# Kernel optimization log

Measured on AMD Instinct MI355X. Metric: run time of the kernel, lower is better.

Reference implementation:

```python
import jax, jax.numpy as jnp
import numpy as np

DILATION = 6
KS = 3
N = KS * KS  # 9 kernel sample points
PAD = 1      # zero padding inside DeformConv2d
EPS = 1e-5


def conv2d(x, w, b=None, padding=0):
    out = jax.lax.conv_general_dilated(
        x, w, window_strides=(1, 1),
        padding=[(padding, padding), (padding, padding)],
        dimension_numbers=('NCHW', 'OIHW', 'NCHW'))
    if b is not None:
        out = out + b[None, :, None, None]
    return out


def batchnorm_train(x, gamma, beta):
    # training-mode BN (module default): batch statistics over (N,H,W)
    mean = x.mean(axis=(0, 2, 3), keepdims=True)
    var = x.var(axis=(0, 2, 3), keepdims=True)
    return gamma[None, :, None, None] * (x - mean) * jax.lax.rsqrt(var + EPS) + beta[None, :, None, None]


def deform_conv(x, p_w, p_b, m_w, m_b, d_w, d_b, w):
    b, c, h, wd = x.shape
    offset = conv2d(x, p_w, p_b, padding=1)                 # (b, 2N, h, w)
    m = jax.nn.sigmoid(conv2d(x, m_w, m_b, padding=1))      # (b, N, h, w) modulation
    s = 2.0 * jax.nn.sigmoid(conv2d(x, d_w, d_b, padding=1))  # (b,1,h,w) adaptive dilation scale (=1 at logit 0)
    xp = jnp.pad(x, ((0, 0), (0, 0), (PAD, PAD), (PAD, PAD)))
    Hp, Wp = h + 2 * PAD, wd + 2 * PAD
    # kernel grid p_n, row-major (kh, kw) to match conv weight layout
    rng = jnp.arange(-(KS - 1) // 2, (KS - 1) // 2 + 1, dtype=x.dtype)
    pn_x, pn_y = jnp.meshgrid(rng, rng, indexing='ij')
    pn_x, pn_y = pn_x.reshape(-1), pn_y.reshape(-1)          # (N,)
    # base sampling positions (offset by PAD into padded map)
    p0_x = jnp.arange(1, h + 1, dtype=x.dtype)[:, None, None]    # (h,1,1)
    p0_y = jnp.arange(1, wd + 1, dtype=x.dtype)[None, :, None]   # (1,w,1)
    off = offset.transpose(0, 2, 3, 1)   # (b,h,w,2N)
    s_ = s.transpose(0, 2, 3, 1)         # (b,h,w,1)
    px = p0_x + DILATION * s_ * pn_x + off[..., :N]   # (b,h,w,N)
    py = p0_y + DILATION * s_ * pn_y + off[..., N:]
    fx, fy = jnp.floor(px), jnp.floor(py)
    qx_lt = jnp.clip(fx, 0, Hp - 1).astype(jnp.int32)
    qy_lt = jnp.clip(fy, 0, Wp - 1).astype(jnp.int32)
    qx_rb = jnp.clip(fx + 1, 0, Hp - 1).astype(jnp.int32)
    qy_rb = jnp.clip(fy + 1, 0, Wp - 1).astype(jnp.int32)
    pxc = jnp.clip(px, 0, Hp - 1)
    pyc = jnp.clip(py, 0, Wp - 1)
    g_lt = (1 + (qx_lt - pxc)) * (1 + (qy_lt - pyc))
    g_rb = (1 - (qx_rb - pxc)) * (1 - (qy_rb - pyc))
    g_lb = (1 + (qx_lt - pxc)) * (1 - (qy_rb - pyc))
    g_rt = (1 - (qx_rb - pxc)) * (1 + (qy_lt - pyc))

    def gather(qx, qy):
        idx = (qx * Wp + qy).reshape(b, 1, -1)                    # (b,1,h*w*N)
        xf = xp.reshape(b, c, Hp * Wp)
        out = jnp.take_along_axis(xf, jnp.broadcast_to(idx, (b, c, idx.shape[-1])), axis=2)
        return out.reshape(b, c, h, wd, N)

    x_off = (g_lt[:, None] * gather(qx_lt, qy_lt)
             + g_rb[:, None] * gather(qx_rb, qy_rb)
             + g_lb[:, None] * gather(qx_lt, qy_rb)
             + g_rt[:, None] * gather(qx_rb, qy_lt))
    x_off = x_off * m.transpose(0, 2, 3, 1)[:, None]              # modulation
    # final 3x3 conv over gathered samples == contraction over (c, N)
    return jnp.einsum('bchwn,ocn->bohw', x_off, w.reshape(w.shape[0], c, N))


def setup_inputs() -> dict:
    key = jax.random.key(0)
    ks = jax.random.split(key, 12)
    cin, c1, c2 = 512, 256, 64
    b, h, w = 2, 96, 96
    def rn(k, shape, scale):
        return jax.random.normal(k, shape, dtype=jnp.float32) * scale
    return {
        'x': rn(ks[0], (b, cin, h, w), 1.0),
        'bn1_g': jnp.ones((cin,), jnp.float32),
        'bn1_b': jnp.zeros((cin,), jnp.float32),
        'conv1_w': rn(ks[1], (c1, cin, 1, 1), (1.0 / cin) ** 0.5),
        'conv1_b': jnp.zeros((c1,), jnp.float32),
        'bn2_g': jnp.ones((c1,), jnp.float32),
        'bn2_b': jnp.zeros((c1,), jnp.float32),
        'p_w': rn(ks[2], (2 * N, c1, 3, 3), 0.01),
        'p_b': jnp.zeros((2 * N,), jnp.float32),
        'm_w': rn(ks[3], (N, c1, 3, 3), 0.01),
        'm_b': jnp.zeros((N,), jnp.float32),
        'd_w': rn(ks[4], (1, c1, 3, 3), 0.01),
        'd_b': jnp.zeros((1,), jnp.float32),
        'dconv_w': rn(ks[5], (c2, c1, 3, 3), (1.0 / (c1 * 9)) ** 0.5),
    }


def reference(x, bn1_g, bn1_b, conv1_w, conv1_b, bn2_g, bn2_b,
              p_w, p_b, m_w, m_b, d_w, d_b, dconv_w):
    f = jax.nn.relu(batchnorm_train(x, bn1_g, bn1_b))
    f = conv2d(f, conv1_w, conv1_b)
    f = batchnorm_train(f, bn2_g, bn2_b)
    return deform_conv(f, p_w, p_b, m_w, m_b, d_w, d_b, dconv_w)
```

## Files before the change

### kernel.cpp

```cpp
#include <hip/hip_runtime.h>
#include <hip/hip_bf16.h>
#include <math.h>

#define BATCH 2
#define CIN 512
#define C1 256
#define C2 64
#define HH 96
#define WW 96
#define HWSZ 9216
#define NPIX 18432
#define HP 98
#define WP 98

typedef __attribute__((ext_vector_type(8))) short bf16x8;
typedef __attribute__((ext_vector_type(4))) short bf16x4;
typedef __attribute__((ext_vector_type(4))) float f32x4;
typedef __attribute__((ext_vector_type(4))) unsigned int u32x4;
typedef __attribute__((ext_vector_type(2))) unsigned int u32x2;
typedef unsigned short u16;
typedef unsigned int u32;

__device__ __forceinline__ float bfu2f(u16 u) {
  u32 v = ((u32)u) << 16; return __builtin_bit_cast(float, v);
}
__device__ __forceinline__ u16 f2bfu(float f) {
  return __builtin_bit_cast(u16, __float2bfloat16(f));
}
__device__ __forceinline__ float rd_any(const void* p, size_t i, int fl) {
  return fl ? bfu2f(((const u16*)p)[i]) : ((const float*)p)[i];
}
__device__ __forceinline__ int get_fl(const u32* g1raw) {
  return g1raw[0] != 0x3F800000u;
}
__device__ __forceinline__ bf16x8 lds_frag(const u16* p) {
  bf16x4 lo = *(const bf16x4*)p;
  bf16x4 hi = *(const bf16x4*)(p + 4);
  bf16x8 r;
  r[0] = lo[0]; r[1] = lo[1]; r[2] = lo[2]; r[3] = lo[3];
  r[4] = hi[0]; r[5] = hi[1]; r[6] = hi[2]; r[7] = hi[3];
  return r;
}
__device__ __forceinline__ void split4(const f32x4& v, u32x2& ph, u32x2& pl) {
  u16 h0 = f2bfu(v[0]), h1 = f2bfu(v[1]), h2 = f2bfu(v[2]), h3 = f2bfu(v[3]);
  u16 l0 = f2bfu(v[0] - bfu2f(h0)), l1 = f2bfu(v[1] - bfu2f(h1));
  u16 l2 = f2bfu(v[2] - bfu2f(h2)), l3 = f2bfu(v[3] - bfu2f(h3));
  ph = (u32x2){(u32)h0 | ((u32)h1 << 16), (u32)h2 | ((u32)h3 << 16)};
  pl = (u32x2){(u32)l0 | ((u32)l1 << 16), (u32)l2 | ((u32)l3 << 16)};
}

#define PREP_BASE 356380
#define NOPART 589824
#define NOUT 1179648
#define NBORD 198656

__global__ __launch_bounds__(256) void prep_kernel(
    const void* cw, const void* pw, const void* mw, const void* dw, const void* dcw,
    const void* cb, const void* g1, const void* b1, const void* g2, const void* b2,
    const void* pb, const void* mb, const void* db,
    u16* __restrict__ W1b, u16* __restrict__ W1l,
    u16* __restrict__ Wofa, u16* __restrict__ Wofal,
    u16* __restrict__ Wab, u16* __restrict__ Wabl,
    float* __restrict__ canon, float* __restrict__ statz,
    float* __restrict__ opartZ, float* __restrict__ oscrZ, void* __restrict__ outZ,
    float* __restrict__ xpfB, int nextra) {
  int e = blockIdx.x * 256 + threadIdx.x;
  if (e >= PREP_BASE + nextra) return;
  int fl = get_fl((const u32*)g1);
  if (e < 131072) {
    float v = rd_any(cw, e, fl);
    u16 h = f2bfu(v);
    W1b[e] = h; W1l[e] = f2bfu(v - bfu2f(h));
  } else if (e < 204800) {
    int i = e - 131072;
    int tap = i >> 13; int r = i & 8191; int m = r >> 8; int c = r & 255;
    float v = 0.f;
    if (m < 18)       v = rd_any(pw, (size_t)(m * 256 + c) * 9 + tap, fl);
    else if (m < 27)  v = rd_any(mw, (size_t)((m - 18) * 256 + c) * 9 + tap, fl);
    else if (m == 27) v = rd_any(dw, (size_t)c * 9 + tap, fl);
    u16 h = f2bfu(v);
    Wofa[i] = h; Wofal[i] = f2bfu(v - bfu2f(h));
  } else if (e < 352256) {
    int i = e - 204800;
    int n = i >> 14; int r = i & 16383; int o = r >> 8; int c = r & 255;
    float v = rd_any(dcw, (size_t)(o * 256 + c) * 9 + n, fl);
    u16 h = f2bfu(v);
    Wab[i] = h; Wabl[i] = f2bfu(v - bfu2f(h));
  } else if (e < 354076) {
    int i = e - 352256;
    const void* src; int off;
    if      (i < 256)  { src = cb; off = i; }
    else if (i < 768)  { src = g1; off = i - 256; }
    else if (i < 1280) { src = b1; off = i - 768; }
    else if (i < 1536) { src = g2; off = i - 1280; }
    else if (i < 1792) { src = b2; off = i - 1536; }
    else if (i < 1810) { src = pb; off = i - 1792; }
    else if (i < 1819) { src = mb; off = i - 1810; }
    else               { src = db; off = i - 1819; }
    canon[i] = rd_any(src, off, fl);
  } else if (e < PREP_BASE) {
    statz[e - 354076] = 0.f;
  } else {
    int k = e - PREP_BASE;
    if (k < NOPART) {
      opartZ[k] = 0.f;
    } else if (k < NOPART + NOUT) {
      int i = k - NOPART;
      if (fl) { ((u16*)outZ)[i] = 0; oscrZ[i] = 0.f; }
      else    { ((float*)outZ)[i] = 0.f; }
    } else {
      int i = k - NOPART - NOUT;
      int ch = i & 255; int pxi = i >> 8;
      int bb = pxi / 388; int r = pxi % 388;
      int h, w;
      if (r < 98)      { h = 0;  w = r; }
      else if (r < 196){ h = 97; w = r - 98; }
      else if (r < 292){ h = r - 196 + 1; w = 0; }
      else             { h = r - 292 + 1; w = 97; }
      xpfB[(((size_t)(bb * HP) + h) * WP + w) * C1 + ch] = 0.f;
    }
  }
}

__global__ __launch_bounds__(256) void init_kernel(
    const u32* __restrict__ g1raw, void* __restrict__ outv,
    float* __restrict__ oscr, float* __restrict__ opart, float* __restrict__ xpf) {
  int i = blockIdx.x * 256 + threadIdx.x;
  if (i < NOUT) {
    if (get_fl(g1raw)) { ((u16*)outv)[i] = 0; oscr[i] = 0.f; }
    else               { ((float*)outv)[i] = 0.f; }
  } else if (i < NOUT + NOPART) {
    opart[i - NOUT] = 0.f;
  } else {
    int k = i - NOUT - NOPART;
    int ch = k & 255; int pxi = k >> 8;
    int bb = pxi / 388; int r = pxi % 388;
    int h, w;
    if (r < 98)      { h = 0;  w = r; }
    else if (r < 196){ h = 97; w = r - 98; }
    else if (r < 292){ h = r - 196 + 1; w = 0; }
    else             { h = r - 292 + 1; w = 97; }
    xpf[(((size_t)(bb * HP) + h) * WP + w) * C1 + ch] = 0.f;
  }
}

__global__ __launch_bounds__(256) void bn_stats_kernel(
    const void* __restrict__ x, const float* __restrict__ gamma,
    const float* __restrict__ beta, float* __restrict__ scale,
    float* __restrict__ shift, float* __restrict__ sums, float* __restrict__ sumsq,
    int* __restrict__ cnt, const u32* __restrict__ g1raw, int C) {
  int c = blockIdx.x, part = blockIdx.y, tid = threadIdx.x;
  int fl = get_fl(g1raw);
  int b = part >> 1, half = part & 1;
  size_t base = ((size_t)(b * C + c)) * HWSZ + half * (HWSZ / 2);
  float s = 0.f, q = 0.f;
  if (fl) {
    const u16* p = (const u16*)x + base;
    for (int i = tid; i < 576; i += 256) {
      u32x4 U = *(const u32x4*)(p + i * 8);
      #pragma unroll
      for (int k = 0; k < 4; ++k) {
        float v0 = bfu2f((u16)(U[k] & 0xffff));
        float v1 = bfu2f((u16)(U[k] >> 16));
        s += v0 + v1; q = fmaf(v0, v0, fmaf(v1, v1, q));
      }
    }
  } else {
    const float* p = (const float*)x + base;
    for (int i = tid; i < 1152; i += 256) {
      f32x4 v = *(const f32x4*)(p + i * 4);
      #pragma unroll
      for (int k = 0; k < 4; ++k) { s += v[k]; q = fmaf(v[k], v[k], q); }
    }
  }
  __shared__ float sh[512];
  sh[tid] = s; sh[tid + 256] = q;
  __syncthreads();
  for (int off = 128; off > 0; off >>= 1) {
    if (tid < off) { sh[tid] += sh[tid + off]; sh[tid + 256] += sh[tid + 256 + off]; }
    __syncthreads();
  }
  if (tid == 0) {
    atomicAdd(&sums[c], sh[0]);
    atomicAdd(&sumsq[c], sh[256]);
    __threadfence();
    int old = atomicAdd(&cnt[c], 1);
    if (old == 3) {
      float S = atomicAdd(&sums[c], 0.f);
      float Q = atomicAdd(&sumsq[c], 0.f);
      float mean = S * (1.f / (float)NPIX);
      float var  = fmaxf(Q * (1.f / (float)NPIX) - mean * mean, 0.f);
      float sc = gamma[c] * rsqrtf(var + 1e-5f);
      scale[c] = sc;
      shift[c] = beta[c] - mean * sc;
    }
  }
}

__global__ __launch_bounds__(256) void conv1x1_kernel(
    const void* __restrict__ x, const u16* __restrict__ W1b, const u16* __restrict__ W1l,
    const float* __restrict__ cb, const float* __restrict__ scale,
    const float* __restrict__ shift, const u32* __restrict__ g1raw,
    u16* __restrict__ f1, float* __restrict__ sums2, float* __restrict__ sumsq2) {
  __shared__ u16 Bh[64][68];
  __shared__ u16 Bl[64][68];
  int tid = threadIdx.x;
  int fl = get_fl(g1raw);
  int bxr = blockIdx.x;
  int bx = (bxr & 7) * 36 + (bxr >> 3);
  int p0 = bx * 64;
  int b = p0 / HWSZ;
  int hw0 = p0 % HWSZ;
  int lane = tid & 63, wv = tid >> 6, quad = lane >> 4, mr = lane & 15;
  int m0 = wv * 64;
  f32x4 acc[4][4];
  #pragma unroll
  for (int i = 0; i < 4; ++i)
    #pragma unroll
    for (int j = 0; j < 4; ++j) acc[i][j] = (f32x4){0.f, 0.f, 0.f, 0.f};

  int spx = tid & 63, cg = tid >> 6;
  int gpx = hw0 + spx;
  for (int c0 = 0; c0 < CIN; c0 += 64) {
    __syncthreads();
    #pragma unroll
    for (int j = 0; j < 8; ++j) {
      int ci = c0 + cg * 16 + j * 2;
      float v0, v1;
      if (fl) {
        const u16* xb = (const u16*)x;
        v0 = bfu2f(xb[((size_t)(b * CIN + ci)) * HWSZ + gpx]);
        v1 = bfu2f(xb[((size_t)(b * CIN + ci + 1)) * HWSZ + gpx]);
      } else {
        const float* xf = (const float*)x;
        v0 = xf[((size_t)(b * CIN + ci)) * HWSZ + gpx];
        v1 = xf[((size_t)(b * CIN + ci + 1)) * HWSZ + gpx];
      }
      v0 = fmaxf(fmaf(v0, scale[ci], shift[ci]), 0.f);
      v1 = fmaxf(fmaf(v1, scale[ci + 1], shift[ci + 1]), 0.f);
      u16 h0 = f2bfu(v0), h1 = f2bfu(v1);
      u16 l0 = f2bfu(v0 - bfu2f(h0)), l1 = f2bfu(v1 - bfu2f(h1));
      *(u32*)&Bh[spx][cg * 16 + j * 2] = (u32)h0 | ((u32)h1 << 16);
      *(u32*)&Bl[spx][cg * 16 + j * 2] = (u32)l0 | ((u32)l1 << 16);
    }
    __syncthreads();
    #pragma unroll
    for (int kk2 = 0; kk2 < 2; ++kk2) {
      int kk = kk2 * 32;
      #pragma unroll
      for (int mf = 0; mf < 4; ++mf) {
        size_t wix = (size_t)(m0 + mf * 16 + mr) * CIN + c0 + kk + quad * 8;
        bf16x8 ah = *(const bf16x8*)(W1b + wix);
        bf16x8 al = *(const bf16x8*)(W1l + wix);
        #pragma unroll
        for (int nt = 0; nt < 4; ++nt) {
          bf16x8 bl = lds_frag(&Bl[nt * 16 + mr][kk + quad * 8]);
          bf16x8 bh = lds_frag(&Bh[nt * 16 + mr][kk + quad * 8]);
          acc[mf][nt] = __builtin_amdgcn_mfma_f32_16x16x32_bf16(ah, bl, acc[mf][nt], 0, 0, 0);
          acc[mf][nt] = __builtin_amdgcn_mfma_f32_16x16x32_bf16(al, bh, acc[mf][nt], 0, 0, 0);
          acc[mf][nt] = __builtin_amdgcn_mfma_f32_16x16x32_bf16(ah, bh, acc[mf][nt], 0, 0, 0);
        }
      }
    }
  }
  #pragma unroll
  for (int mf = 0; mf < 4; ++mf) {
    #pragma unroll
    for (int r = 0; r < 4; ++r) {
      int co = m0 + mf * 16 + quad * 4 + r;
      float bi = cb[co];
      float sv = 0.f, sq = 0.f;
      #pragma unroll
      for (int nt = 0; nt < 4; ++nt) {
        float v = acc[mf][nt][r] + bi;
        f1[((size_t)(b * C1 + co)) * HWSZ + hw0 + nt * 16 + mr] = f2bfu(v);
        sv += v; sq = fmaf(v, v, sq);
      }
      #pragma unroll
      for (int m = 1; m < 16; m <<= 1) {
        sv += __shfl_xor(sv, m);
        sq += __shfl_xor(sq, m);
      }
      if (mr == 0) {
        atomicAdd(&sums2[co], sv);
        atomicAdd(&sumsq2[co], sq);
      }
    }
  }
}

__global__ __launch_bounds__(256) void bn2pad_kernel(
    const u16* __restrict__ f1, const float* __restrict__ sums2,
    const float* __restrict__ sumsq2, const float* __restrict__ g2c,
    const float* __restrict__ b2c, float* __restrict__ xpf) {
  int bid = blockIdx.x;
  int ht = bid % 144; int ct = (bid / 144) & 3; int b = bid / 576;
  int hw0 = ht * 64, c0 = ct * 64;
  __shared__ float t[64][65];
  __shared__ float s2[64], sh2[64];
  int tid = threadIdx.x;
  if (tid < 64) {
    int c = c0 + tid;
    float S = sums2[c], Q = sumsq2[c];
    float mean = S * (1.f / (float)NPIX);
    float var  = fmaxf(Q * (1.f / (float)NPIX) - mean * mean, 0.f);
    float sc = g2c[c] * rsqrtf(var + 1e-5f);
    s2[tid] = sc;
    sh2[tid] = b2c[c] - mean * sc;
  }
  __syncthreads();
  #pragma unroll
  for (int it = 0; it < 16; ++it) {
    int e = it * 256 + tid;
    int p = e & 63, ci = e >> 6;
    float v = bfu2f(f1[((size_t)(b * C1 + c0 + ci)) * HWSZ + hw0 + p]);
    t[ci][p] = fmaf(v, s2[ci], sh2[ci]);
  }
  __syncthreads();
  #pragma unroll
  for (int it = 0; it < 16; ++it) {
    int e = it * 256 + tid;
    int ci = e & 63, p = e >> 6;
    int hw = hw0 + p; int h = hw / WW; int w = hw % WW;
    xpf[(((size_t)(b * HP) + h + 1) * WP + w + 1) * C1 + c0 + ci] = t[ci][p];
  }
}

__global__ __launch_bounds__(256) void offconv_kernel(
    const float* __restrict__ xpf, const u16* __restrict__ Wofa, const u16* __restrict__ Wofal,
    const float* __restrict__ pbc, const float* __restrict__ mbc,
    const float* __restrict__ dbc, float* __restrict__ opart) {
  __shared__ u16 Vh[32][68];
  __shared__ u16 Vl[32][68];
  int tid = threadIdx.x;
  int bxr = blockIdx.x;
  int bx = (bxr & 7) * 72 + (bxr >> 3);
  int tg = blockIdx.y;
  int p0 = bx * 32;
  int b = p0 / HWSZ;
  int hw = p0 % HWSZ; int h0 = hw / WW; int w0 = hw % WW;
  int lane = tid & 63, wv = tid >> 6, quad = lane >> 4, mr = lane & 15;
  int m0 = (wv & 1) * 16;
  int ntile = wv >> 1;
  int srow = tid >> 4;
  int scol = (tid & 15) * 4;
  f32x4 acc = (f32x4){0.f, 0.f, 0.f, 0.f};
  for (int tt = 0; tt < 3; ++tt) {
    int tap = tg * 3 + tt;
    int th = tap / 3, tw = tap % 3;
    const float* base = xpf + ((size_t)(b * HP + h0 + th) * WP + (w0 + tw)) * C1;
    for (int c0i = 0; c0i < 4; ++c0i) {
      int c0 = c0i * 64;
      if (tt | c0i) __syncthreads();
      #pragma unroll
      for (int pass = 0; pass < 2; ++pass) {
        int px = pass * 16 + srow;
        f32x4 v = *(const f32x4*)(base + (size_t)px * C1 + c0 + scol);
        u32x2 ph, pl;
        split4(v, ph, pl);
        *(u32x2*)&Vh[px][scol] = ph;
        *(u32x2*)&Vl[px][scol] = pl;
      }
      __syncthreads();
      #pragma unroll
      for (int kk2 = 0; kk2 < 2; ++kk2) {
        int kof = kk2 * 32 + quad * 8;
        size_t wix = (size_t)(tap * 32 + m0 + mr) * C1 + c0 + kof;
        bf16x8 ah = *(const bf16x8*)(Wofa + wix);
        bf16x8 al = *(const bf16x8*)(Wofal + wix);
        bf16x8 bl = lds_frag(&Vl[ntile * 16 + mr][kof]);
        bf16x8 bh = lds_frag(&Vh[ntile * 16 + mr][kof]);
        acc = __builtin_amdgcn_mfma_f32_16x16x32_bf16(ah, bl, acc, 0, 0, 0);
        acc = __builtin_amdgcn_mfma_f32_16x16x32_bf16(al, bh, acc, 0, 0, 0);
        acc = __builtin_amdgcn_mfma_f32_16x16x32_bf16(ah, bh, acc, 0, 0, 0);
      }
    }
  }
  int px = ntile * 16 + mr;
  #pragma unroll
  for (int r = 0; r < 4; ++r) {
    int m = m0 + quad * 4 + r;
    if (m < 28) {
      float v = acc[r];
      if (tg == 0) v += (m < 18) ? pbc[m] : ((m < 27) ? mbc[m - 18] : dbc[0]);
      atomicAdd(&opart[(size_t)m * NPIX + p0 + px], v);
    }
  }
}

__global__ __launch_bounds__(256) void deform_kernel(
    const float* __restrict__ xpf, const u16* __restrict__ Wab, const u16* __restrict__ Wabl,
    const float* __restrict__ opart, const u32* __restrict__ g1raw,
    float* __restrict__ oscr, void* __restrict__ outv) {
  __shared__ u16   Vh[64][68];
  __shared__ u16   Vl[64][68];
  __shared__ int   smi[4][64];
  __shared__ float smw[4][64];
  int tid = threadIdx.x;
  int bxr = blockIdx.x;
  int bx = (bxr & 7) * 36 + (bxr >> 3);
  int n = blockIdx.y;
  int p0 = bx * 64;
  int b = p0 / HWSZ;
  int hw0 = p0 % HWSZ;

  if (tid < 64) {
    int p = tid;
    int bp = p0 + p;
    int hw = hw0 + p; int h = hw / WW; int w = hw % WW;
    float offx = opart[(size_t)n * NPIX + bp];
    float offy = opart[(size_t)(9 + n) * NPIX + bp];
    float mlog = opart[(size_t)(18 + n) * NPIX + bp];
    float slog = opart[(size_t)27 * NPIX + bp];
    float mm = 1.f / (1.f + expf(-mlog));
    float s  = 2.f / (1.f + expf(-slog));
    float pnx = (float)(n / 3 - 1), pny = (float)(n % 3 - 1);
    float px = (float)(h + 1) + 6.f * s * pnx + offx;
    float py = (float)(w + 1) + 6.f * s * pny + offy;
    float fx = floorf(px), fy = floorf(py);
    float qxlt = fminf(fmaxf(fx, 0.f), 97.f);
    float qylt = fminf(fmaxf(fy, 0.f), 97.f);
    float qxrb = fminf(fmaxf(fx + 1.f, 0.f), 97.f);
    float qyrb = fminf(fmaxf(fy + 1.f, 0.f), 97.f);
    float pxc = fminf(fmaxf(px, 0.f), 97.f);
    float pyc = fminf(fmaxf(py, 0.f), 97.f);
    float glt = (1.f + (qxlt - pxc)) * (1.f + (qylt - pyc));
    float grb = (1.f - (qxrb - pxc)) * (1.f - (qyrb - pyc));
    float glb = (1.f + (qxlt - pxc)) * (1.f - (qyrb - pyc));
    float grt = (1.f - (qxrb - pxc)) * (1.f + (qylt - pyc));
    int ixlt = (int)qxlt, iylt = (int)qylt, ixrb = (int)qxrb, iyrb = (int)qyrb;
    int base = b * (HP * WP);
    smi[0][p] = base + ixlt * WP + iylt;  smw[0][p] = glt * mm;
    smi[1][p] = base + ixrb * WP + iyrb;  smw[1][p] = grb * mm;
    smi[2][p] = base + ixlt * WP + iyrb;  smw[2][p] = glb * mm;
    smi[3][p] = base + ixrb * WP + iylt;  smw[3][p] = grt * mm;
  }
  __syncthreads();

  int lane = tid & 63, wv = tid >> 6, quad = lane >> 4, mr = lane & 15;
  int m0 = wv * 16;
  int srow = tid >> 4;
  int scol = (tid & 15) * 4;
  f32x4 acc[4];
  #pragma unroll
  for (int i = 0; i < 4; ++i) acc[i] = (f32x4){0.f, 0.f, 0.f, 0.f};

  const float* bp[4][4];
  float wt[4][4];
  #pragma unroll
  for (int pass = 0; pass < 4; ++pass) {
    int px = pass * 16 + srow;
    #pragma unroll
    for (int c = 0; c < 4; ++c) {
      bp[pass][c] = xpf + (size_t)smi[c][px] * C1 + scol;
      wt[pass][c] = smw[c][px];
    }
  }
  f32x4 pv[4][4];
  #pragma unroll
  for (int pass = 0; pass < 4; ++pass)
    #pragma unroll
    for (int c = 0; c < 4; ++c) pv[pass][c] = *(const f32x4*)(bp[pass][c]);

  for (int c0i = 0; c0i < 4; ++c0i) {
    int c0 = c0i * 64;
    if (c0i) __syncthreads();
    #pragma unroll
    for (int pass = 0; pass < 4; ++pass) {
      int px = pass * 16 + srow;
      f32x4 vc;
      #pragma unroll
      for (int j = 0; j < 4; ++j)
        vc[j] = fmaf(wt[pass][0], pv[pass][0][j],
                 fmaf(wt[pass][1], pv[pass][1][j],
                  fmaf(wt[pass][2], pv[pass][2][j], wt[pass][3] * pv[pass][3][j])));
      u32x2 ph, pl;
      split4(vc, ph, pl);
      *(u32x2*)&Vh[px][scol] = ph;
      *(u32x2*)&Vl[px][scol] = pl;
    }
    __syncthreads();
    if (c0i < 3) {
      int cn = c0 + 64;
      #pragma unroll
      for (int pass = 0; pass < 4; ++pass)
        #pragma unroll
        for (int c = 0; c < 4; ++c) pv[pass][c] = *(const f32x4*)(bp[pass][c] + cn);
    }
    #pragma unroll
    for (int kk2 = 0; kk2 < 2; ++kk2) {
      int kof = kk2 * 32 + quad * 8;
      size_t wix = (size_t)(n * C2 + m0 + mr) * C1 + c0 + kof;
      bf16x8 ah = *(const bf16x8*)(Wab + wix);
      bf16x8 al = *(const bf16x8*)(Wabl + wix);
      #pragma unroll
      for (int nt = 0; nt < 4; ++nt) {
        bf16x8 bl = lds_frag(&Vl[nt * 16 + mr][kof]);
        bf16x8 bh = lds_frag(&Vh[nt * 16 + mr][kof]);
        acc[nt] = __builtin_amdgcn_mfma_f32_16x16x32_bf16(ah, bl, acc[nt], 0, 0, 0);
        acc[nt] = __builtin_amdgcn_mfma_f32_16x16x32_bf16(al, bh, acc[nt], 0, 0, 0);
        acc[nt] = __builtin_amdgcn_mfma_f32_16x16x32_bf16(ah, bh, acc[nt], 0, 0, 0);
      }
    }
  }
  int fl = get_fl(g1raw);
  float* tgt = fl ? oscr : (float*)outv;
  #pragma unroll
  for (int nt = 0; nt < 4; ++nt) {
    #pragma unroll
    for (int r = 0; r < 4; ++r) {
      int o = m0 + quad * 4 + r;
      int hw = hw0 + nt * 16 + mr;
      atomicAdd(&tgt[((size_t)(b * C2 + o)) * HWSZ + hw], acc[nt][r]);
    }
  }
}

__global__ void cvt_out_kernel(const u32* __restrict__ g1raw,
                               const float* __restrict__ oscr, void* __restrict__ outv) {
  if (!get_fl(g1raw)) return;
  int i = blockIdx.x * 256 + threadIdx.x;
  ((u16*)outv)[i] = f2bfu(oscr[i]);
}

extern "C" void kernel_launch(void* const* d_in, const int* in_sizes, int n_in,
                              void* d_out, int out_size, void* d_ws, size_t ws_size,
                              hipStream_t stream) {
  const void* x       = d_in[0];
  const void* bn1_g   = d_in[1];
  const void* bn1_b   = d_in[2];
  const void* conv1_w = d_in[3];
  const void* conv1_b = d_in[4];
  const void* bn2_g   = d_in[5];
  const void* bn2_b   = d_in[6];
  const void* p_w     = d_in[7];
  const void* p_b     = d_in[8];
  const void* m_w     = d_in[9];
  const void* m_b     = d_in[10];
  const void* d_w     = d_in[11];
  const void* d_b     = d_in[12];
  const void* dconv_w = d_in[13];
  const u32* g1raw = (const u32*)bn1_g;

  float* ws = (float*)d_ws;
  float* canon = ws + 16;
  float* cbc = canon + 0;
  float* g1c = canon + 256;
  float* b1c = canon + 768;
  float* g2c = canon + 1280;
  float* b2c = canon + 1536;
  float* pbc = canon + 1792;
  float* mbc = canon + 1810;
  float* dbc = canon + 1819;
  float* scale1 = ws + 1840;
  float* shift1 = ws + 2352;
  float* statz  = ws + 3376;
  float* sums1  = statz;
  float* sumsq1 = statz + 512;
  int*   cnt1   = (int*)(statz + 1024);
  float* sums2  = statz + 1536;
  float* sumsq2 = statz + 1792;
  u16* W1b   = (u16*)(ws + 5680);
  u16* W1l   = (u16*)(ws + 71216);
  u16* Wofa  = (u16*)(ws + 136752);
  u16* Wofal = (u16*)(ws + 173616);
  u16* Wab   = (u16*)(ws + 210480);
  u16* Wabl  = (u16*)(ws + 284208);
  u16* f1    = (u16*)(ws + 357936);

  bool bigws = ws_size >= (size_t)9403952 * 4 + 64;
  float *opart, *oscr, *xpf;
  if (bigws) {
    opart = ws + 2717232;
    oscr  = ws + 3307056;
    xpf   = ws + 4486704;
  } else {
    oscr  = ws + 357936;
    opart = ws + 1537584;
    xpf   = ws + 2717232;
  }

  prep_kernel<<<bigws ? 9081 : 1393, 256, 0, stream>>>(
      conv1_w, p_w, m_w, d_w, dconv_w,
      conv1_b, bn1_g, bn1_b, bn2_g, bn2_b, p_b, m_b, d_b,
      W1b, W1l, Wofa, Wofal, Wab, Wabl, canon, statz,
      opart, oscr, d_out, xpf, bigws ? (NOPART + NOUT + NBORD) : 0);
  bn_stats_kernel<<<dim3(CIN, 4), 256, 0, stream>>>(x, g1c, b1c, scale1, shift1,
                                                    sums1, sumsq1, cnt1, g1raw, CIN);
  conv1x1_kernel<<<288, 256, 0, stream>>>(x, W1b, W1l, cbc, scale1, shift1, g1raw,
                                          f1, sums2, sumsq2);
  bn2pad_kernel<<<1152, 256, 0, stream>>>(f1, sums2, sumsq2, g2c, b2c, xpf);
  if (!bigws)
    init_kernel<<<(NOUT + NOPART + NBORD + 255) / 256, 256, 0, stream>>>(
        g1raw, d_out, oscr, opart, xpf);
  offconv_kernel<<<dim3(576, 3), 256, 0, stream>>>(xpf, Wofa, Wofal, pbc, mbc, dbc, opart);
  deform_kernel<<<dim3(288, 9), 256, 0, stream>>>(xpf, Wab, Wabl, opart, g1raw, oscr, d_out);
  cvt_out_kernel<<<4608, 256, 0, stream>>>(g1raw, oscr, d_out);
}
```

Measured before the change: 339.0 us.

## Retile conv1x1 into smaller blocks with register prefetch; share offconv tap row loads

The 1x1 conv kernel now uses 32-pixel by 128-channel tiles on a 2D grid of 576x2 blocks, four times the previous block count, to raise occupancy. It also prefetches the next input channel slab into registers while the MFMAs run. The offset conv kernel loads one 34-row strip per kernel row and reuses it for all three horizontal taps with shifted LDS reads, which cuts global loads and barriers. In exchange, the conv1x1 input activations are read twice (once per channel half), and more atomics are issued for the BN2 statistics.

```diff
diff --git a/kernel.cpp b/kernel.cpp
--- a/kernel.cpp
+++ b/kernel.cpp
@@ -202,64 +202,68 @@
     const float* __restrict__ cb, const float* __restrict__ scale,
     const float* __restrict__ shift, const u32* __restrict__ g1raw,
     u16* __restrict__ f1, float* __restrict__ sums2, float* __restrict__ sumsq2) {
-  __shared__ u16 Bh[64][68];
-  __shared__ u16 Bl[64][68];
+  __shared__ u16 Bh[32][68];
+  __shared__ u16 Bl[32][68];
   int tid = threadIdx.x;
   int fl = get_fl(g1raw);
   int bxr = blockIdx.x;
-  int bx = (bxr & 7) * 36 + (bxr >> 3);
-  int p0 = bx * 64;
+  int bx = (bxr & 7) * 72 + (bxr >> 3);
+  int p0 = bx * 32;
   int b = p0 / HWSZ;
   int hw0 = p0 % HWSZ;
   int lane = tid & 63, wv = tid >> 6, quad = lane >> 4, mr = lane & 15;
-  int m0 = wv * 64;
-  f32x4 acc[4][4];
-  #pragma unroll
-  for (int i = 0; i < 4; ++i)
-    #pragma unroll
-    for (int j = 0; j < 4; ++j) acc[i][j] = (f32x4){0.f, 0.f, 0.f, 0.f};
-
-  int spx = tid & 63, cg = tid >> 6;
+  int m0 = blockIdx.y * 128 + (wv & 1) * 64;
+  int nt = wv >> 1;
+  f32x4 acc[4];
+  #pragma unroll
+  for (int j = 0; j < 4; ++j) acc[j] = (f32x4){0.f, 0.f, 0.f, 0.f};
+
+  int spx = tid & 31, cg = tid >> 5;
   int gpx = hw0 + spx;
-  for (int c0 = 0; c0 < CIN; c0 += 64) {
-    __syncthreads();
-    #pragma unroll
-    for (int j = 0; j < 8; ++j) {
-      int ci = c0 + cg * 16 + j * 2;
-      float v0, v1;
-      if (fl) {
-        const u16* xb = (const u16*)x;
-        v0 = bfu2f(xb[((size_t)(b * CIN + ci)) * HWSZ + gpx]);
-        v1 = bfu2f(xb[((size_t)(b * CIN + ci + 1)) * HWSZ + gpx]);
-      } else {
-        const float* xf = (const float*)x;
-        v0 = xf[((size_t)(b * CIN + ci)) * HWSZ + gpx];
-        v1 = xf[((size_t)(b * CIN + ci + 1)) * HWSZ + gpx];
-      }
-      v0 = fmaxf(fmaf(v0, scale[ci], shift[ci]), 0.f);
-      v1 = fmaxf(fmaf(v1, scale[ci + 1], shift[ci + 1]), 0.f);
+  const u16* xb = (const u16*)x;
+  const float* xf = (const float*)x;
+  float xv[8];
+  #pragma unroll
+  for (int j = 0; j < 8; ++j) {
+    int ci = cg * 8 + j;
+    xv[j] = fl ? bfu2f(xb[((size_t)(b * CIN + ci)) * HWSZ + gpx])
+               : xf[((size_t)(b * CIN + ci)) * HWSZ + gpx];
+  }
+  for (int c0i = 0; c0i < 8; ++c0i) {
+    int c0 = c0i * 64;
+    if (c0i) __syncthreads();
+    #pragma unroll
+    for (int j = 0; j < 4; ++j) {
+      int ci = c0 + cg * 8 + j * 2;
+      float v0 = fmaxf(fmaf(xv[j * 2], scale[ci], shift[ci]), 0.f);
+      float v1 = fmaxf(fmaf(xv[j * 2 + 1], scale[ci + 1], shift[ci + 1]), 0.f);
       u16 h0 = f2bfu(v0), h1 = f2bfu(v1);
       u16 l0 = f2bfu(v0 - bfu2f(h0)), l1 = f2bfu(v1 - bfu2f(h1));
-      *(u32*)&Bh[spx][cg * 16 + j * 2] = (u32)h0 | ((u32)h1 << 16);
-      *(u32*)&Bl[spx][cg * 16 + j * 2] = (u32)l0 | ((u32)l1 << 16);
+      *(u32*)&Bh[spx][cg * 8 + j * 2] = (u32)h0 | ((u32)h1 << 16);
+      *(u32*)&Bl[spx][cg * 8 + j * 2] = (u32)l0 | ((u32)l1 << 16);
     }
     __syncthreads();
+    if (c0i < 7) {
+      #pragma unroll
+      for (int j = 0; j < 8; ++j) {
+        int ci = c0 + 64 + cg * 8 + j;
+        xv[j] = fl ? bfu2f(xb[((size_t)(b * CIN + ci)) * HWSZ + gpx])
+                   : xf[((size_t)(b * CIN + ci)) * HWSZ + gpx];
+      }
+    }
     #pragma unroll
     for (int kk2 = 0; kk2 < 2; ++kk2) {
-      int kk = kk2 * 32;
+      int kof = kk2 * 32 + quad * 8;
+      bf16x8 bl = lds_frag(&Bl[nt * 16 + mr][kof]);
+      bf16x8 bh = lds_frag(&Bh[nt * 16 + mr][kof]);
       #pragma unroll
       for (int mf = 0; mf < 4; ++mf) {
-        size_t wix = (size_t)(m0 + mf * 16 + mr) * CIN + c0 + kk + quad * 8;
+        size_t wix = (size_t)(m0 + mf * 16 + mr) * CIN + c0 + kof;
         bf16x8 ah = *(const bf16x8*)(W1b + wix);
         bf16x8 al = *(const bf16x8*)(W1l + wix);
-        #pragma unroll
-        for (int nt = 0; nt < 4; ++nt) {
-          bf16x8 bl = lds_frag(&Bl[nt * 16 + mr][kk + quad * 8]);
-          bf16x8 bh = lds_frag(&Bh[nt * 16 + mr][kk + quad * 8]);
-          acc[mf][nt] = __builtin_amdgcn_mfma_f32_16x16x32_bf16(ah, bl, acc[mf][nt], 0, 0, 0);
-          acc[mf][nt] = __builtin_amdgcn_mfma_f32_16x16x32_bf16(al, bh, acc[mf][nt], 0, 0, 0);
-          acc[mf][nt] = __builtin_amdgcn_mfma_f32_16x16x32_bf16(ah, bh, acc[mf][nt], 0, 0, 0);
-        }
+        acc[mf] = __builtin_amdgcn_mfma_f32_16x16x32_bf16(ah, bl, acc[mf], 0, 0, 0);
+        acc[mf] = __builtin_amdgcn_mfma_f32_16x16x32_bf16(al, bh, acc[mf], 0, 0, 0);
+        acc[mf] = __builtin_amdgcn_mfma_f32_16x16x32_bf16(ah, bh, acc[mf], 0, 0, 0);
       }
     }
   }
@@ -268,14 +272,9 @@
     #pragma unroll
     for (int r = 0; r < 4; ++r) {
       int co = m0 + mf * 16 + quad * 4 + r;
-      float bi = cb[co];
-      float sv = 0.f, sq = 0.f;
-      #pragma unroll
-      for (int nt = 0; nt < 4; ++nt) {
-        float v = acc[mf][nt][r] + bi;
-        f1[((size_t)(b * C1 + co)) * HWSZ + hw0 + nt * 16 + mr] = f2bfu(v);
-        sv += v; sq = fmaf(v, v, sq);
-      }
+      float v = acc[mf][r] + cb[co];
+      f1[((size_t)(b * C1 + co)) * HWSZ + hw0 + nt * 16 + mr] = f2bfu(v);
+      float sv = v, sq = v * v;
       #pragma unroll
       for (int m = 1; m < 16; m <<= 1) {
         sv += __shfl_xor(sv, m);
@@ -330,8 +329,8 @@
     const float* __restrict__ xpf, const u16* __restrict__ Wofa, const u16* __restrict__ Wofal,
     const float* __restrict__ pbc, const float* __restrict__ mbc,
     const float* __restrict__ dbc, float* __restrict__ opart) {
-  __shared__ u16 Vh[32][68];
-  __shared__ u16 Vl[32][68];
+  __shared__ u16 Vh[34][68];
+  __shared__ u16 Vl[34][68];
   int tid = threadIdx.x;
   int bxr = blockIdx.x;
   int bx = (bxr & 7) * 72 + (bxr >> 3);
@@ -344,32 +343,34 @@
   int ntile = wv >> 1;
   int srow = tid >> 4;
   int scol = (tid & 15) * 4;
+  const float* base = xpf + ((size_t)(b * HP + h0 + tg) * WP + w0) * C1;
   f32x4 acc = (f32x4){0.f, 0.f, 0.f, 0.f};
-  for (int tt = 0; tt < 3; ++tt) {
-    int tap = tg * 3 + tt;
-    int th = tap / 3, tw = tap % 3;
-    const float* base = xpf + ((size_t)(b * HP + h0 + th) * WP + (w0 + tw)) * C1;
-    for (int c0i = 0; c0i < 4; ++c0i) {
-      int c0 = c0i * 64;
-      if (tt | c0i) __syncthreads();
-      #pragma unroll
-      for (int pass = 0; pass < 2; ++pass) {
-        int px = pass * 16 + srow;
-        f32x4 v = *(const f32x4*)(base + (size_t)px * C1 + c0 + scol);
+  for (int c0i = 0; c0i < 4; ++c0i) {
+    int c0 = c0i * 64;
+    if (c0i) __syncthreads();
+    #pragma unroll
+    for (int pass = 0; pass < 3; ++pass) {
+      int r = pass * 16 + srow;
+      if (pass < 2 || srow < 2) {
+        f32x4 v = *(const f32x4*)(base + (size_t)r * C1 + c0 + scol);
         u32x2 ph, pl;
         split4(v, ph, pl);
-        *(u32x2*)&Vh[px][scol] = ph;
-        *(u32x2*)&Vl[px][scol] = pl;
-      }
-      __syncthreads();
+        *(u32x2*)&Vh[r][scol] = ph;
+        *(u32x2*)&Vl[r][scol] = pl;
+      }
+    }
+    __syncthreads();
+    #pragma unroll
+    for (int tt = 0; tt < 3; ++tt) {
+      int tap = tg * 3 + tt;
       #pragma unroll
       for (int kk2 = 0; kk2 < 2; ++kk2) {
         int kof = kk2 * 32 + quad * 8;
         size_t wix = (size_t)(tap * 32 + m0 + mr) * C1 + c0 + kof;
         bf16x8 ah = *(const bf16x8*)(Wofa + wix);
         bf16x8 al = *(const bf16x8*)(Wofal + wix);
-        bf16x8 bl = lds_frag(&Vl[ntile * 16 + mr][kof]);
-        bf16x8 bh = lds_frag(&Vh[ntile * 16 + mr][kof]);
+        bf16x8 bl = lds_frag(&Vl[tt + ntile * 16 + mr][kof]);
+        bf16x8 bh = lds_frag(&Vh[tt + ntile * 16 + mr][kof]);
         acc = __builtin_amdgcn_mfma_f32_16x16x32_bf16(ah, bl, acc, 0, 0, 0);
         acc = __builtin_amdgcn_mfma_f32_16x16x32_bf16(al, bh, acc, 0, 0, 0);
         acc = __builtin_amdgcn_mfma_f32_16x16x32_bf16(ah, bh, acc, 0, 0, 0);
@@ -587,8 +588,8 @@
       opart, oscr, d_out, xpf, bigws ? (NOPART + NOUT + NBORD) : 0);
   bn_stats_kernel<<<dim3(CIN, 4), 256, 0, stream>>>(x, g1c, b1c, scale1, shift1,
                                                     sums1, sumsq1, cnt1, g1raw, CIN);
-  conv1x1_kernel<<<288, 256, 0, stream>>>(x, W1b, W1l, cbc, scale1, shift1, g1raw,
-                                          f1, sums2, sumsq2);
+  conv1x1_kernel<<<dim3(576, 2), 256, 0, stream>>>(x, W1b, W1l, cbc, scale1, shift1, g1raw,
+                                                   f1, sums2, sumsq2);
   bn2pad_kernel<<<1152, 256, 0, stream>>>(f1, sums2, sumsq2, g2c, b2c, xpf);
   if (!bigws)
     init_kernel<<<(NOUT + NOPART + NBORD + 255) / 256, 256, 0, stream>>>(
```

After: 542.9 us. 1.6x slower.
